# Kernel optimization log

Measured on AMD Instinct MI355X. Metric: run time of the kernel, lower is better.

The kernel has to match this reference:

```python
import jax, jax.numpy as jnp
import numpy as np

NUM_RAYS = 262144  # 512x512 image
NUM_SAMPLES = 64


def setup_inputs() -> dict:
    key = jax.random.key(0)
    k1, k2 = jax.random.split(key)
    rays_o = jax.random.normal(k1, (NUM_RAYS, 3), dtype=jnp.float32) * 0.1
    d = jax.random.normal(k2, (NUM_RAYS, 3), dtype=jnp.float32)
    rays_d = d / jnp.linalg.norm(d, axis=-1, keepdims=True)
    radii = jnp.full((1,), 1.3, dtype=jnp.float32)  # scene_radii buffer
    return {"rays_o": rays_o, "rays_d": rays_d, "radii": radii, "num_samples": NUM_SAMPLES}


def _raymarch_dense(rays_o, rays_d, radii, num_samples):
    # Ray-AABB (cube of half-extent radius) intersection + depth linspace.
    radius = radii[0]
    inv_d = 1.0 / jnp.where(rays_d == 0, jnp.full_like(rays_d, 1e-6), rays_d)
    off_neg = (-radius - rays_o) * inv_d
    off_pos = (radius - rays_o) * inv_d
    near = jnp.max(jnp.minimum(off_neg, off_pos), axis=-1, keepdims=True)  # [N,1]
    far = jnp.min(jnp.maximum(off_neg, off_pos), axis=-1, keepdims=True)   # [N,1]
    t = jnp.linspace(0.0, 1.0, num_samples, dtype=rays_o.dtype)[None]       # [1,S]
    depth = near + (far - near) * t                                         # [N,S]
    # perturb=False path (deterministic)
    samples = (rays_o[:, None, :] + rays_d[:, None, :] * depth[..., None]) / radius  # [N,S,3]
    deltas = jnp.diff(depth, axis=-1, prepend=near)                          # [N,S]
    # Concrete query_mask: occupied = inside unit sphere of normalized grid.
    mask = jnp.linalg.norm(samples, axis=-1) <= 1.0                          # [N,S] bool
    return samples, depth, deltas, mask


def reference(rays_o, rays_d, radii, num_samples):
    n = rays_o.shape[0]
    samples, depth, deltas, mask = _raymarch_dense(rays_o, rays_d, radii, num_samples)
    M = n * num_samples
    mf = mask.reshape(M)
    # Stable compaction: valid entries first, original order preserved (jnp.argsort is stable).
    order = jnp.argsort(jnp.logical_not(mf))
    num_valid = jnp.sum(mf).astype(jnp.int32)
    ridx_full = jnp.repeat(jnp.arange(n, dtype=jnp.int32), num_samples)
    ridx = ridx_full[order]                                  # [M]
    samples_c = samples.reshape(M, 3)[order]                 # [M,3]
    depth_c = depth.reshape(M)[order]                        # [M]
    deltas_c = deltas.reshape(M)[order][:, None]             # [M,1]
    valid = jnp.arange(M) < num_valid                        # padding indicator
    # mark_pack_boundaries: start of each per-ray pack
    boundary = jnp.concatenate([jnp.ones((1,), bool), ridx[1:] != ridx[:-1]]) & valid
    return ridx, samples_c, depth_c, deltas_c, boundary, num_valid
```

## Files before the change

### kernel.cpp

```cpp
#include <hip/hip_runtime.h>

#pragma clang fp contract(off)

namespace {

constexpr int S = 64;
constexpr float DELTA = 1.0f / 63.0f;

constexpr int RPB = 8;
constexpr int TPR = 256 / RPB;
constexpr int SPT = S / TPR;
constexpr int Q = RPB * S;
constexpr int LQ = Q + 16;
constexpr int SB = 4 * LQ;
constexpr int LDSF = SB + 3 * Q + 16;

__device__ __forceinline__ void ray_nearfar(
    float ox, float oy, float oz,
    float dx, float dy, float dz,
    float R, float& nr, float& fr) {
  float ix = 1.0f / ((dx == 0.0f) ? 1e-6f : dx);
  float iy = 1.0f / ((dy == 0.0f) ? 1e-6f : dy);
  float iz = 1.0f / ((dz == 0.0f) ? 1e-6f : dz);
  float mR = -R;
  float ax = (mR - ox) * ix, bx = (R - ox) * ix;
  float ay = (mR - oy) * iy, by = (R - oy) * iy;
  float az = (mR - oz) * iz, bz = (R - oz) * iz;
  nr = fmaxf(fmaxf(fminf(ax, bx), fminf(ay, by)), fminf(az, bz));
  fr = fminf(fminf(fmaxf(ax, bx), fmaxf(ay, by)), fmaxf(az, bz));
}

__global__ __launch_bounds__(256) void k_count(
    const float* __restrict__ ro, const float* __restrict__ rd,
    const float* __restrict__ radii,
    float4* __restrict__ rayinfo,
    int* __restrict__ L, int* __restrict__ blockSums, int N) {
  int r = blockIdx.x * 256 + threadIdx.x;
  int cnt = 0;
  const float QLIM = __uint_as_float(0x3F800001u);
  if (r < N) {
    float R = radii[0];
    float ox = ro[3 * r], oy = ro[3 * r + 1], oz = ro[3 * r + 2];
    float dx = rd[3 * r], dy = rd[3 * r + 1], dz = rd[3 * r + 2];
    float nr, fr;
    ray_nearfar(ox, oy, oz, dx, dy, dz, R, nr, fr);
    float f = fr - nr;
    unsigned lo = 0, hi = 0;
    for (int s = 0; s < S; ++s) {
      float dep = nr + f * ((float)s * DELTA);
      float sx = (ox + dx * dep) / R;
      float sy = (oy + dy * dep) / R;
      float sz = (oz + dz * dep) / R;
      float q = (sx * sx + sy * sy) + sz * sz;
      unsigned bit = (q <= QLIM) ? 1u : 0u;
      if (s < 32) lo |= bit << s; else hi |= bit << (s - 32);
      cnt += (int)bit;
    }
    rayinfo[r] = make_float4(nr, f, __uint_as_float(lo), __uint_as_float(hi));
  }
  __shared__ int sm[256];
  sm[threadIdx.x] = cnt;
  __syncthreads();
  for (int off = 1; off < 256; off <<= 1) {
    int t = (threadIdx.x >= off) ? sm[threadIdx.x - off] : 0;
    __syncthreads();
    sm[threadIdx.x] += t;
    __syncthreads();
  }
  if (r < N) L[r] = sm[threadIdx.x] - cnt;
  if (threadIdx.x == 255) blockSums[blockIdx.x] = sm[255];
}

__global__ __launch_bounds__(1024) void k_scan(
    const int* __restrict__ blockSums, int* __restrict__ blockOff,
    int* __restrict__ total, float* __restrict__ out_nv, int nb) {
  __shared__ int sm[1024];
  int x = (threadIdx.x < nb) ? blockSums[threadIdx.x] : 0;
  sm[threadIdx.x] = x;
  __syncthreads();
  for (int off = 1; off < 1024; off <<= 1) {
    int t = (threadIdx.x >= off) ? sm[threadIdx.x - off] : 0;
    __syncthreads();
    sm[threadIdx.x] += t;
    __syncthreads();
  }
  if (threadIdx.x < nb) blockOff[threadIdx.x] = sm[threadIdx.x] - x;
  if (threadIdx.x == 1023) {
    *total = sm[1023];
    out_nv[0] = (float)sm[1023];
  }
}

__global__ __launch_bounds__(256) void k_stage(
    const float* __restrict__ ro, const float* __restrict__ rd,
    const float* __restrict__ radii,
    const float4* __restrict__ rayinfo,
    const int* __restrict__ L, const int* __restrict__ blockOff,
    const int* __restrict__ total,
    float* __restrict__ out, int N) {
  __shared__ __align__(16) float buf[LDSF];
  int nwg = gridDim.x;
  int chunk = nwg >> 3;
  int hw = blockIdx.x;
  int bid = (hw & 7) * chunk + (hw >> 3);
  int r0 = bid * RPB;
  int tid = threadIdx.x;
  int nv = *total;
  int V0 = L[r0] + blockOff[r0 >> 8];
  int rB = r0 + RPB;
  int VB = (rB >= N) ? nv : (L[rB] + blockOff[rB >> 8]);
  int cV = VB - V0;
  int cT = Q - cV;
  int TV = r0 * S - V0;
  size_t tail0 = (size_t)nv + (size_t)TV;

  int sv = V0 & 3;
  int st = ((sv + cV + 3) & ~3) + (int)(tail0 & 3);
  int svS = (3 * V0) & 3;
  int stS = ((svS + 3 * cV + 3) & ~3) + (int)((3 * tail0) & 3);

  int r = r0 + (tid / TPR);
  float R = radii[0];
  float invR = 1.0f / R;
  float4 info = rayinfo[r];
  float nr = info.x, f = info.y;
  unsigned long long msk =
      ((unsigned long long)__float_as_uint(info.w) << 32) |
      (unsigned long long)__float_as_uint(info.z);
  float ox = ro[3 * r], oy = ro[3 * r + 1], oz = ro[3 * r + 2];
  float dx = rd[3 * r], dy = rd[3 * r + 1], dz = rd[3 * r + 2];
  int Vr = L[r] + blockOff[r >> 8];
  float fridx = (float)r;
  int idxvB = Vr - V0;
  int idxtB = (r * S - Vr) - TV;
  #pragma unroll
  for (int j = 0; j < SPT; ++j) {
    int s = (tid & (TPR - 1)) + TPR * j;
    bool bit = (msk >> s) & 1ull;
    int below = __popcll(msk & ((1ull << s) - 1ull));
    float dep = fmaf(f, (float)s * DELTA, nr);
    float sx = fmaf(dx, dep, ox) * invR;
    float sy = fmaf(dy, dep, oy) * invR;
    float sz = fmaf(dz, dep, oz) * invR;
    float prev = fmaf(f, (float)(s - 1) * DELTA, nr);
    float del = s ? (dep - prev) : 0.0f;
    int i1 = bit ? (idxvB + below) : (idxtB + (s - below));
    int b0 = (bit ? sv : st) + i1;
    buf[b0] = fridx;
    buf[b0 + LQ] = dep;
    buf[b0 + 2 * LQ] = del;
    buf[b0 + 3 * LQ] = (bit && below == 0) ? 1.0f : 0.0f;
    int b1 = SB + (bit ? svS : stS) + 3 * i1;
    buf[b1] = sx; buf[b1 + 1] = sy; buf[b1 + 2] = sz;
  }
  __syncthreads();

  size_t M = (size_t)N * S;
  const size_t A1 = 4 * M, A2 = 5 * M, A3 = 6 * M;

  {
    int a0 = (-V0) & 3; if (a0 > cV) a0 = cV;
    int body = cV - a0, n4 = body >> 2, rem = body & 3;
    int l0 = sv + a0;
    size_t g = (size_t)V0 + a0;
    for (int c = tid; c < n4; c += 256) {
      int l = l0 + 4 * c; size_t gg = g + 4 * (size_t)c;
      *(float4*)(out + gg)      = *(const float4*)&buf[l];
      *(float4*)(out + A1 + gg) = *(const float4*)&buf[l + LQ];
      *(float4*)(out + A2 + gg) = *(const float4*)&buf[l + 2 * LQ];
      *(float4*)(out + A3 + gg) = *(const float4*)&buf[l + 3 * LQ];
    }
    if (tid < a0) {
      size_t gg = (size_t)V0 + tid; int l = sv + tid;
      out[gg] = buf[l]; out[A1 + gg] = buf[l + LQ];
      out[A2 + gg] = buf[l + 2 * LQ]; out[A3 + gg] = buf[l + 3 * LQ];
    }
    if (tid < rem) {
      int e = a0 + 4 * n4 + tid;
      size_t gg = (size_t)V0 + e; int l = sv + e;
      out[gg] = buf[l]; out[A1 + gg] = buf[l + LQ];
      out[A2 + gg] = buf[l + 2 * LQ]; out[A3 + gg] = buf[l + 3 * LQ];
    }
  }
  {
    int a0 = (int)((-tail0) & 3); if (a0 > cT) a0 = cT;
    int body = cT - a0, n4 = body >> 2, rem = body & 3;
    int l0 = st + a0;
    size_t g = tail0 + a0;
    for (int c = tid; c < n4; c += 256) {
      int l = l0 + 4 * c; size_t gg = g + 4 * (size_t)c;
      *(float4*)(out + gg)      = *(const float4*)&buf[l];
      *(float4*)(out + A1 + gg) = *(const float4*)&buf[l + LQ];
      *(float4*)(out + A2 + gg) = *(const float4*)&buf[l + 2 * LQ];
      *(float4*)(out + A3 + gg) = *(const float4*)&buf[l + 3 * LQ];
    }
    if (tid < a0) {
      size_t gg = tail0 + tid; int l = st + tid;
      out[gg] = buf[l]; out[A1 + gg] = buf[l + LQ];
      out[A2 + gg] = buf[l + 2 * LQ]; out[A3 + gg] = buf[l + 3 * LQ];
    }
    if (tid < rem) {
      int e = a0 + 4 * n4 + tid;
      size_t gg = tail0 + e; int l = st + e;
      out[gg] = buf[l]; out[A1 + gg] = buf[l + LQ];
      out[A2 + gg] = buf[l + 2 * LQ]; out[A3 + gg] = buf[l + 3 * LQ];
    }
  }
  {
    size_t g0 = M + 3 * (size_t)V0; int cnt = 3 * cV;
    int a0 = (int)((-g0) & 3); if (a0 > cnt) a0 = cnt;
    int body = cnt - a0, n4 = body >> 2, rem = body & 3;
    int l0 = SB + svS + a0;
    for (int c = tid; c < n4; c += 256)
      *(float4*)(out + g0 + a0 + 4 * (size_t)c) = *(const float4*)&buf[l0 + 4 * c];
    if (tid < a0) out[g0 + tid] = buf[SB + svS + tid];
    if (tid < rem) { int e = a0 + 4 * n4 + tid; out[g0 + e] = buf[SB + svS + e]; }
  }
  {
    size_t g0 = M + 3 * tail0; int cnt = 3 * cT;
    int a0 = (int)((-g0) & 3); if (a0 > cnt) a0 = cnt;
    int body = cnt - a0, n4 = body >> 2, rem = body & 3;
    int l0 = SB + stS + a0;
    for (int c = tid; c < n4; c += 256)
      *(float4*)(out + g0 + a0 + 4 * (size_t)c) = *(const float4*)&buf[l0 + 4 * c];
    if (tid < a0) out[g0 + tid] = buf[SB + stS + tid];
    if (tid < rem) { int e = a0 + 4 * n4 + tid; out[g0 + e] = buf[SB + stS + e]; }
  }
}

}

extern "C" void kernel_launch(void* const* d_in, const int* in_sizes, int n_in,
                              void* d_out, int out_size, void* d_ws, size_t ws_size,
                              hipStream_t stream) {
  const float* ro = (const float*)d_in[0];
  const float* rd = (const float*)d_in[1];
  const float* radii = (const float*)d_in[2];
  int N = in_sizes[0] / 3;
  int M = N * S;
  int nbA = (N + 255) / 256;

  float4* rayinfo = (float4*)d_ws;
  int* wsI = (int*)(rayinfo + N);
  int* L = wsI;
  int* blockSums = wsI + N;
  int* blockOff = blockSums + nbA;
  int* total = blockOff + nbA;

  float* out = (float*)d_out;
  float* out_nv = out + (size_t)7 * (size_t)M;

  k_count<<<nbA, 256, 0, stream>>>(ro, rd, radii, rayinfo, L, blockSums, N);
  k_scan<<<1, 1024, 0, stream>>>(blockSums, blockOff, total, out_nv, nbA);
  k_stage<<<N / RPB, 256, 0, stream>>>(ro, rd, radii, rayinfo, L, blockOff,
                                       total, out, N);
}
```

Before: 139.1 us.

## Make staging kernel persistent with double-buffered LDS and prefetch; fast-path mask test

The staging kernel becomes persistent: 512 blocks each loop over several 16-ray chunks. Each block uses two LDS buffers and prefetches the next chunk's ray data while the current chunk is written out, to hide global load latency and cut launch and block-scheduling overhead. The count kernel now tests the sphere mask with FMA and a reciprocal multiply, and falls back to the exact division path only near the boundary, which reduces division cost. The risks are fewer resident blocks with larger LDS, losing the XCD-aware block remapping, and cpb truncation if the chunk count is not divisible by 512. The persistent loop also has a single barrier per chunk, so a chunk can overwrite the buffer from two chunks ago while slower threads may still be reading it.

```diff
diff --git a/kernel.cpp b/kernel.cpp
--- a/kernel.cpp
+++ b/kernel.cpp
@@ -7,13 +7,14 @@
 constexpr int S = 64;
 constexpr float DELTA = 1.0f / 63.0f;
 
-constexpr int RPB = 8;
+constexpr int RPB = 16;
 constexpr int TPR = 256 / RPB;
 constexpr int SPT = S / TPR;
 constexpr int Q = RPB * S;
 constexpr int LQ = Q + 16;
 constexpr int SB = 4 * LQ;
 constexpr int LDSF = SB + 3 * Q + 16;
+constexpr int NBLK = 512;
 
 __device__ __forceinline__ void ray_nearfar(
     float ox, float oy, float oz,
@@ -40,6 +41,7 @@
   const float QLIM = __uint_as_float(0x3F800001u);
   if (r < N) {
     float R = radii[0];
+    float invR = 1.0f / R;
     float ox = ro[3 * r], oy = ro[3 * r + 1], oz = ro[3 * r + 2];
     float dx = rd[3 * r], dy = rd[3 * r + 1], dz = rd[3 * r + 2];
     float nr, fr;
@@ -48,11 +50,20 @@
     unsigned lo = 0, hi = 0;
     for (int s = 0; s < S; ++s) {
       float dep = nr + f * ((float)s * DELTA);
-      float sx = (ox + dx * dep) / R;
-      float sy = (oy + dy * dep) / R;
-      float sz = (oz + dz * dep) / R;
-      float q = (sx * sx + sy * sy) + sz * sz;
-      unsigned bit = (q <= QLIM) ? 1u : 0u;
+      float sxf = fmaf(dx, dep, ox) * invR;
+      float syf = fmaf(dy, dep, oy) * invR;
+      float szf = fmaf(dz, dep, oz) * invR;
+      float qf = fmaf(sxf, sxf, fmaf(syf, syf, szf * szf));
+      unsigned bit;
+      if (__builtin_expect(fabsf(qf - 1.0f) > 6e-5f, 1)) {
+        bit = (qf <= 1.0f) ? 1u : 0u;
+      } else {
+        float sx = (ox + dx * dep) / R;
+        float sy = (oy + dy * dep) / R;
+        float sz = (oz + dz * dep) / R;
+        float q = (sx * sx + sy * sy) + sz * sz;
+        bit = (q <= QLIM) ? 1u : 0u;
+      }
       if (s < 32) lo |= bit << s; else hi |= bit << (s - 32);
       cnt += (int)bit;
     }
@@ -91,140 +102,162 @@
   }
 }
 
-__global__ __launch_bounds__(256) void k_stage(
+__global__ __launch_bounds__(256, 2) void k_stage(
     const float* __restrict__ ro, const float* __restrict__ rd,
     const float* __restrict__ radii,
     const float4* __restrict__ rayinfo,
     const int* __restrict__ L, const int* __restrict__ blockOff,
     const int* __restrict__ total,
-    float* __restrict__ out, int N) {
-  __shared__ __align__(16) float buf[LDSF];
-  int nwg = gridDim.x;
-  int chunk = nwg >> 3;
-  int hw = blockIdx.x;
-  int bid = (hw & 7) * chunk + (hw >> 3);
-  int r0 = bid * RPB;
-  int tid = threadIdx.x;
-  int nv = *total;
+    float* __restrict__ out, int N, int cpb) {
+  __shared__ __align__(16) float buf[2][LDSF];
+  const int tid = threadIdx.x;
+  const int nv = *total;
+  const float R = radii[0];
+  const float invR = 1.0f / R;
+  const size_t M = (size_t)N * S;
+  const size_t A1 = 4 * M, A2 = 5 * M, A3 = 6 * M;
+
+  int c0 = blockIdx.x * cpb;
+  int r0 = c0 * RPB;
   int V0 = L[r0] + blockOff[r0 >> 8];
   int rB = r0 + RPB;
   int VB = (rB >= N) ? nv : (L[rB] + blockOff[rB >> 8]);
-  int cV = VB - V0;
-  int cT = Q - cV;
-  int TV = r0 * S - V0;
-  size_t tail0 = (size_t)nv + (size_t)TV;
-
-  int sv = V0 & 3;
-  int st = ((sv + cV + 3) & ~3) + (int)(tail0 & 3);
-  int svS = (3 * V0) & 3;
-  int stS = ((svS + 3 * cV + 3) & ~3) + (int)((3 * tail0) & 3);
-
-  int r = r0 + (tid / TPR);
-  float R = radii[0];
-  float invR = 1.0f / R;
+  int r = r0 + (tid >> 4);
   float4 info = rayinfo[r];
-  float nr = info.x, f = info.y;
-  unsigned long long msk =
-      ((unsigned long long)__float_as_uint(info.w) << 32) |
-      (unsigned long long)__float_as_uint(info.z);
   float ox = ro[3 * r], oy = ro[3 * r + 1], oz = ro[3 * r + 2];
   float dx = rd[3 * r], dy = rd[3 * r + 1], dz = rd[3 * r + 2];
   int Vr = L[r] + blockOff[r >> 8];
-  float fridx = (float)r;
-  int idxvB = Vr - V0;
-  int idxtB = (r * S - Vr) - TV;
-  #pragma unroll
-  for (int j = 0; j < SPT; ++j) {
-    int s = (tid & (TPR - 1)) + TPR * j;
-    bool bit = (msk >> s) & 1ull;
-    int below = __popcll(msk & ((1ull << s) - 1ull));
-    float dep = fmaf(f, (float)s * DELTA, nr);
-    float sx = fmaf(dx, dep, ox) * invR;
-    float sy = fmaf(dy, dep, oy) * invR;
-    float sz = fmaf(dz, dep, oz) * invR;
-    float prev = fmaf(f, (float)(s - 1) * DELTA, nr);
-    float del = s ? (dep - prev) : 0.0f;
-    int i1 = bit ? (idxvB + below) : (idxtB + (s - below));
-    int b0 = (bit ? sv : st) + i1;
-    buf[b0] = fridx;
-    buf[b0 + LQ] = dep;
-    buf[b0 + 2 * LQ] = del;
-    buf[b0 + 3 * LQ] = (bit && below == 0) ? 1.0f : 0.0f;
-    int b1 = SB + (bit ? svS : stS) + 3 * i1;
-    buf[b1] = sx; buf[b1 + 1] = sy; buf[b1 + 2] = sz;
-  }
-  __syncthreads();
-
-  size_t M = (size_t)N * S;
-  const size_t A1 = 4 * M, A2 = 5 * M, A3 = 6 * M;
-
-  {
-    int a0 = (-V0) & 3; if (a0 > cV) a0 = cV;
-    int body = cV - a0, n4 = body >> 2, rem = body & 3;
-    int l0 = sv + a0;
-    size_t g = (size_t)V0 + a0;
-    for (int c = tid; c < n4; c += 256) {
-      int l = l0 + 4 * c; size_t gg = g + 4 * (size_t)c;
-      *(float4*)(out + gg)      = *(const float4*)&buf[l];
-      *(float4*)(out + A1 + gg) = *(const float4*)&buf[l + LQ];
-      *(float4*)(out + A2 + gg) = *(const float4*)&buf[l + 2 * LQ];
-      *(float4*)(out + A3 + gg) = *(const float4*)&buf[l + 3 * LQ];
-    }
-    if (tid < a0) {
-      size_t gg = (size_t)V0 + tid; int l = sv + tid;
-      out[gg] = buf[l]; out[A1 + gg] = buf[l + LQ];
-      out[A2 + gg] = buf[l + 2 * LQ]; out[A3 + gg] = buf[l + 3 * LQ];
-    }
-    if (tid < rem) {
-      int e = a0 + 4 * n4 + tid;
-      size_t gg = (size_t)V0 + e; int l = sv + e;
-      out[gg] = buf[l]; out[A1 + gg] = buf[l + LQ];
-      out[A2 + gg] = buf[l + 2 * LQ]; out[A3 + gg] = buf[l + 3 * LQ];
-    }
-  }
-  {
-    int a0 = (int)((-tail0) & 3); if (a0 > cT) a0 = cT;
-    int body = cT - a0, n4 = body >> 2, rem = body & 3;
-    int l0 = st + a0;
-    size_t g = tail0 + a0;
-    for (int c = tid; c < n4; c += 256) {
-      int l = l0 + 4 * c; size_t gg = g + 4 * (size_t)c;
-      *(float4*)(out + gg)      = *(const float4*)&buf[l];
-      *(float4*)(out + A1 + gg) = *(const float4*)&buf[l + LQ];
-      *(float4*)(out + A2 + gg) = *(const float4*)&buf[l + 2 * LQ];
-      *(float4*)(out + A3 + gg) = *(const float4*)&buf[l + 3 * LQ];
-    }
-    if (tid < a0) {
-      size_t gg = tail0 + tid; int l = st + tid;
-      out[gg] = buf[l]; out[A1 + gg] = buf[l + LQ];
-      out[A2 + gg] = buf[l + 2 * LQ]; out[A3 + gg] = buf[l + 3 * LQ];
-    }
-    if (tid < rem) {
-      int e = a0 + 4 * n4 + tid;
-      size_t gg = tail0 + e; int l = st + e;
-      out[gg] = buf[l]; out[A1 + gg] = buf[l + LQ];
-      out[A2 + gg] = buf[l + 2 * LQ]; out[A3 + gg] = buf[l + 3 * LQ];
-    }
-  }
-  {
-    size_t g0 = M + 3 * (size_t)V0; int cnt = 3 * cV;
-    int a0 = (int)((-g0) & 3); if (a0 > cnt) a0 = cnt;
-    int body = cnt - a0, n4 = body >> 2, rem = body & 3;
-    int l0 = SB + svS + a0;
-    for (int c = tid; c < n4; c += 256)
-      *(float4*)(out + g0 + a0 + 4 * (size_t)c) = *(const float4*)&buf[l0 + 4 * c];
-    if (tid < a0) out[g0 + tid] = buf[SB + svS + tid];
-    if (tid < rem) { int e = a0 + 4 * n4 + tid; out[g0 + e] = buf[SB + svS + e]; }
-  }
-  {
-    size_t g0 = M + 3 * tail0; int cnt = 3 * cT;
-    int a0 = (int)((-g0) & 3); if (a0 > cnt) a0 = cnt;
-    int body = cnt - a0, n4 = body >> 2, rem = body & 3;
-    int l0 = SB + stS + a0;
-    for (int c = tid; c < n4; c += 256)
-      *(float4*)(out + g0 + a0 + 4 * (size_t)c) = *(const float4*)&buf[l0 + 4 * c];
-    if (tid < a0) out[g0 + tid] = buf[SB + stS + tid];
-    if (tid < rem) { int e = a0 + 4 * n4 + tid; out[g0 + e] = buf[SB + stS + e]; }
+
+  for (int k = 0; k < cpb; ++k) {
+    float* bufp = buf[k & 1];
+    bool has_next = (k + 1 < cpb);
+    float4 n_info; float n_ox, n_oy, n_oz, n_dx, n_dy, n_dz;
+    int n_Vr = 0, n_VB = 0, n_r0 = 0;
+    if (has_next) {
+      n_r0 = (c0 + k + 1) * RPB;
+      int rr = n_r0 + (tid >> 4);
+      n_info = rayinfo[rr];
+      n_ox = ro[3 * rr]; n_oy = ro[3 * rr + 1]; n_oz = ro[3 * rr + 2];
+      n_dx = rd[3 * rr]; n_dy = rd[3 * rr + 1]; n_dz = rd[3 * rr + 2];
+      n_Vr = L[rr] + blockOff[rr >> 8];
+      int nrB = n_r0 + RPB;
+      n_VB = (nrB >= N) ? nv : (L[nrB] + blockOff[nrB >> 8]);
+    }
+
+    int cV = VB - V0;
+    int cT = Q - cV;
+    int TV = r0 * S - V0;
+    size_t tail0 = (size_t)nv + (size_t)TV;
+    int sv = V0 & 3;
+    int st = ((sv + cV + 3) & ~3) + (int)(tail0 & 3);
+    int svS = (3 * V0) & 3;
+    int stS = ((svS + 3 * cV + 3) & ~3) + (int)((3 * tail0) & 3);
+
+    float nr = info.x, f = info.y;
+    unsigned long long msk =
+        ((unsigned long long)__float_as_uint(info.w) << 32) |
+        (unsigned long long)__float_as_uint(info.z);
+    float fridx = (float)(r0 + (tid >> 4));
+    int rr = r0 + (tid >> 4);
+    int idxvB = Vr - V0;
+    int idxtB = (rr * S - Vr) - TV;
+    #pragma unroll
+    for (int j = 0; j < SPT; ++j) {
+      int s = (tid & (TPR - 1)) + TPR * j;
+      bool bit = (msk >> s) & 1ull;
+      int below = __popcll(msk & ((1ull << s) - 1ull));
+      float dep = fmaf(f, (float)s * DELTA, nr);
+      float sx = fmaf(dx, dep, ox) * invR;
+      float sy = fmaf(dy, dep, oy) * invR;
+      float sz = fmaf(dz, dep, oz) * invR;
+      float prev = fmaf(f, (float)(s - 1) * DELTA, nr);
+      float del = s ? (dep - prev) : 0.0f;
+      int i1 = bit ? (idxvB + below) : (idxtB + (s - below));
+      int b0 = (bit ? sv : st) + i1;
+      bufp[b0] = fridx;
+      bufp[b0 + LQ] = dep;
+      bufp[b0 + 2 * LQ] = del;
+      bufp[b0 + 3 * LQ] = (bit && below == 0) ? 1.0f : 0.0f;
+      int b1 = SB + (bit ? svS : stS) + 3 * i1;
+      bufp[b1] = sx; bufp[b1 + 1] = sy; bufp[b1 + 2] = sz;
+    }
+    __syncthreads();
+
+    {
+      int a0 = (-V0) & 3; if (a0 > cV) a0 = cV;
+      int body = cV - a0, n4 = body >> 2, rem = body & 3;
+      int l0 = sv + a0;
+      size_t g = (size_t)V0 + a0;
+      for (int c = tid; c < n4; c += 256) {
+        int l = l0 + 4 * c; size_t gg = g + 4 * (size_t)c;
+        *(float4*)(out + gg)      = *(const float4*)&bufp[l];
+        *(float4*)(out + A1 + gg) = *(const float4*)&bufp[l + LQ];
+        *(float4*)(out + A2 + gg) = *(const float4*)&bufp[l + 2 * LQ];
+        *(float4*)(out + A3 + gg) = *(const float4*)&bufp[l + 3 * LQ];
+      }
+      if (tid < a0) {
+        size_t gg = (size_t)V0 + tid; int l = sv + tid;
+        out[gg] = bufp[l]; out[A1 + gg] = bufp[l + LQ];
+        out[A2 + gg] = bufp[l + 2 * LQ]; out[A3 + gg] = bufp[l + 3 * LQ];
+      }
+      if (tid < rem) {
+        int e = a0 + 4 * n4 + tid;
+        size_t gg = (size_t)V0 + e; int l = sv + e;
+        out[gg] = bufp[l]; out[A1 + gg] = bufp[l + LQ];
+        out[A2 + gg] = bufp[l + 2 * LQ]; out[A3 + gg] = bufp[l + 3 * LQ];
+      }
+    }
+    {
+      int a0 = (int)((-tail0) & 3); if (a0 > cT) a0 = cT;
+      int body = cT - a0, n4 = body >> 2, rem = body & 3;
+      int l0 = st + a0;
+      size_t g = tail0 + a0;
+      for (int c = tid; c < n4; c += 256) {
+        int l = l0 + 4 * c; size_t gg = g + 4 * (size_t)c;
+        *(float4*)(out + gg)      = *(const float4*)&bufp[l];
+        *(float4*)(out + A1 + gg) = *(const float4*)&bufp[l + LQ];
+        *(float4*)(out + A2 + gg) = *(const float4*)&bufp[l + 2 * LQ];
+        *(float4*)(out + A3 + gg) = *(const float4*)&bufp[l + 3 * LQ];
+      }
+      if (tid < a0) {
+        size_t gg = tail0 + tid; int l = st + tid;
+        out[gg] = bufp[l]; out[A1 + gg] = bufp[l + LQ];
+        out[A2 + gg] = bufp[l + 2 * LQ]; out[A3 + gg] = bufp[l + 3 * LQ];
+      }
+      if (tid < rem) {
+        int e = a0 + 4 * n4 + tid;
+        size_t gg = tail0 + e; int l = st + e;
+        out[gg] = bufp[l]; out[A1 + gg] = bufp[l + LQ];
+        out[A2 + gg] = bufp[l + 2 * LQ]; out[A3 + gg] = bufp[l + 3 * LQ];
+      }
+    }
+    {
+      size_t g0 = M + 3 * (size_t)V0; int cnt = 3 * cV;
+      int a0 = (int)((-g0) & 3); if (a0 > cnt) a0 = cnt;
+      int body = cnt - a0, n4 = body >> 2, rem = body & 3;
+      int l0 = SB + svS + a0;
+      for (int c = tid; c < n4; c += 256)
+        *(float4*)(out + g0 + a0 + 4 * (size_t)c) = *(const float4*)&bufp[l0 + 4 * c];
+      if (tid < a0) out[g0 + tid] = bufp[SB + svS + tid];
+      if (tid < rem) { int e = a0 + 4 * n4 + tid; out[g0 + e] = bufp[SB + svS + e]; }
+    }
+    {
+      size_t g0 = M + 3 * tail0; int cnt = 3 * cT;
+      int a0 = (int)((-g0) & 3); if (a0 > cnt) a0 = cnt;
+      int body = cnt - a0, n4 = body >> 2, rem = body & 3;
+      int l0 = SB + stS + a0;
+      for (int c = tid; c < n4; c += 256)
+        *(float4*)(out + g0 + a0 + 4 * (size_t)c) = *(const float4*)&bufp[l0 + 4 * c];
+      if (tid < a0) out[g0 + tid] = bufp[SB + stS + tid];
+      if (tid < rem) { int e = a0 + 4 * n4 + tid; out[g0 + e] = bufp[SB + stS + e]; }
+    }
+
+    if (has_next) {
+      r0 = n_r0; V0 = VB; VB = n_VB;
+      info = n_info; Vr = n_Vr;
+      ox = n_ox; oy = n_oy; oz = n_oz;
+      dx = n_dx; dy = n_dy; dz = n_dz;
+    }
   }
 }
 
@@ -239,6 +272,8 @@
   int N = in_sizes[0] / 3;
   int M = N * S;
   int nbA = (N + 255) / 256;
+  int chunks = N / RPB;
+  int cpb = chunks / NBLK;
 
   float4* rayinfo = (float4*)d_ws;
   int* wsI = (int*)(rayinfo + N);
@@ -252,6 +287,6 @@
 
   k_count<<<nbA, 256, 0, stream>>>(ro, rd, radii, rayinfo, L, blockSums, N);
   k_scan<<<1, 1024, 0, stream>>>(blockSums, blockOff, total, out_nv, nbA);
-  k_stage<<<N / RPB, 256, 0, stream>>>(ro, rd, radii, rayinfo, L, blockOff,
-                                       total, out, N);
-}
+  k_stage<<<NBLK, 256, 0, stream>>>(ro, rd, radii, rayinfo, L, blockOff,
+                                    total, out, N, cpb);
+}
```

Result: slower. 154.9 us (+11.3%).

## Fuse block-sum scan into count kernel, add fast FMA mask test, double rays per block

Applied to the files above, without the earlier changes.

Removes the separate single-block scan kernel. The last count block to finish, detected through an atomic counter, now scans the block sums itself. The per-sample inside-sphere test uses FMA and a reciprocal multiply, falling back to the exact division path only when the value lies near the boundary. The staging kernel handles 16 rays per block instead of 8. This adds a memset launch, and the 256-thread last-block scan covers only up to 1024 block sums.

```diff
diff --git a/kernel.cpp b/kernel.cpp
--- a/kernel.cpp
+++ b/kernel.cpp
@@ -7,7 +7,7 @@
 constexpr int S = 64;
 constexpr float DELTA = 1.0f / 63.0f;
 
-constexpr int RPB = 8;
+constexpr int RPB = 16;
 constexpr int TPR = 256 / RPB;
 constexpr int SPT = S / TPR;
 constexpr int Q = RPB * S;
@@ -34,12 +34,15 @@
     const float* __restrict__ ro, const float* __restrict__ rd,
     const float* __restrict__ radii,
     float4* __restrict__ rayinfo,
-    int* __restrict__ L, int* __restrict__ blockSums, int N) {
+    int* __restrict__ L, int* __restrict__ blockSums,
+    int* __restrict__ blockOff, int* __restrict__ total,
+    float* __restrict__ out_nv, int* __restrict__ counter, int N) {
   int r = blockIdx.x * 256 + threadIdx.x;
   int cnt = 0;
   const float QLIM = __uint_as_float(0x3F800001u);
   if (r < N) {
     float R = radii[0];
+    float invR = 1.0f / R;
     float ox = ro[3 * r], oy = ro[3 * r + 1], oz = ro[3 * r + 2];
     float dx = rd[3 * r], dy = rd[3 * r + 1], dz = rd[3 * r + 2];
     float nr, fr;
@@ -48,11 +51,20 @@
     unsigned lo = 0, hi = 0;
     for (int s = 0; s < S; ++s) {
       float dep = nr + f * ((float)s * DELTA);
-      float sx = (ox + dx * dep) / R;
-      float sy = (oy + dy * dep) / R;
-      float sz = (oz + dz * dep) / R;
-      float q = (sx * sx + sy * sy) + sz * sz;
-      unsigned bit = (q <= QLIM) ? 1u : 0u;
+      float sxf = fmaf(dx, dep, ox) * invR;
+      float syf = fmaf(dy, dep, oy) * invR;
+      float szf = fmaf(dz, dep, oz) * invR;
+      float qf = fmaf(sxf, sxf, fmaf(syf, syf, szf * szf));
+      unsigned bit;
+      if (__builtin_expect(fabsf(qf - 1.0f) > 6e-5f, 1)) {
+        bit = (qf <= 1.0f) ? 1u : 0u;
+      } else {
+        float sx = (ox + dx * dep) / R;
+        float sy = (oy + dy * dep) / R;
+        float sz = (oz + dz * dep) / R;
+        float q = (sx * sx + sy * sy) + sz * sz;
+        bit = (q <= QLIM) ? 1u : 0u;
+      }
       if (s < 32) lo |= bit << s; else hi |= bit << (s - 32);
       cnt += (int)bit;
     }
@@ -69,25 +81,38 @@
   }
   if (r < N) L[r] = sm[threadIdx.x] - cnt;
   if (threadIdx.x == 255) blockSums[blockIdx.x] = sm[255];
-}
-
-__global__ __launch_bounds__(1024) void k_scan(
-    const int* __restrict__ blockSums, int* __restrict__ blockOff,
-    int* __restrict__ total, float* __restrict__ out_nv, int nb) {
-  __shared__ int sm[1024];
-  int x = (threadIdx.x < nb) ? blockSums[threadIdx.x] : 0;
-  sm[threadIdx.x] = x;
-  __syncthreads();
-  for (int off = 1; off < 1024; off <<= 1) {
-    int t = (threadIdx.x >= off) ? sm[threadIdx.x - off] : 0;
-    __syncthreads();
-    sm[threadIdx.x] += t;
-    __syncthreads();
-  }
-  if (threadIdx.x < nb) blockOff[threadIdx.x] = sm[threadIdx.x] - x;
-  if (threadIdx.x == 1023) {
-    *total = sm[1023];
-    out_nv[0] = (float)sm[1023];
+
+  __threadfence();
+  __shared__ int lastFlag;
+  if (threadIdx.x == 0)
+    lastFlag = (atomicAdd(counter, 1) == (int)gridDim.x - 1) ? 1 : 0;
+  __syncthreads();
+  if (!lastFlag) return;
+
+  int nb = (int)gridDim.x;
+  int base = threadIdx.x * 4;
+  int v0 = (base + 0 < nb) ? atomicAdd(&blockSums[base + 0], 0) : 0;
+  int v1 = (base + 1 < nb) ? atomicAdd(&blockSums[base + 1], 0) : 0;
+  int v2 = (base + 2 < nb) ? atomicAdd(&blockSums[base + 2], 0) : 0;
+  int v3 = (base + 3 < nb) ? atomicAdd(&blockSums[base + 3], 0) : 0;
+  int s1 = v0 + v1, s2 = s1 + v2, s3 = s2 + v3;
+  __shared__ int sm2[256];
+  sm2[threadIdx.x] = s3;
+  __syncthreads();
+  for (int off = 1; off < 256; off <<= 1) {
+    int t = (threadIdx.x >= off) ? sm2[threadIdx.x - off] : 0;
+    __syncthreads();
+    sm2[threadIdx.x] += t;
+    __syncthreads();
+  }
+  int excl = sm2[threadIdx.x] - s3;
+  if (base + 0 < nb) blockOff[base + 0] = excl;
+  if (base + 1 < nb) blockOff[base + 1] = excl + v0;
+  if (base + 2 < nb) blockOff[base + 2] = excl + s1;
+  if (base + 3 < nb) blockOff[base + 3] = excl + s2;
+  if (threadIdx.x == 255) {
+    *total = sm2[255];
+    out_nv[0] = (float)sm2[255];
   }
 }
 
@@ -119,7 +144,7 @@
   int svS = (3 * V0) & 3;
   int stS = ((svS + 3 * cV + 3) & ~3) + (int)((3 * tail0) & 3);
 
-  int r = r0 + (tid / TPR);
+  int r = r0 + (tid >> 4);
   float R = radii[0];
   float invR = 1.0f / R;
   float4 info = rayinfo[r];
@@ -246,12 +271,14 @@
   int* blockSums = wsI + N;
   int* blockOff = blockSums + nbA;
   int* total = blockOff + nbA;
+  int* counter = total + 1;
 
   float* out = (float*)d_out;
   float* out_nv = out + (size_t)7 * (size_t)M;
 
-  k_count<<<nbA, 256, 0, stream>>>(ro, rd, radii, rayinfo, L, blockSums, N);
-  k_scan<<<1, 1024, 0, stream>>>(blockSums, blockOff, total, out_nv, nbA);
+  hipMemsetAsync(counter, 0, sizeof(int), stream);
+  k_count<<<nbA, 256, 0, stream>>>(ro, rd, radii, rayinfo, L, blockSums,
+                                   blockOff, total, out_nv, counter, N);
   k_stage<<<N / RPB, 256, 0, stream>>>(ro, rd, radii, rayinfo, L, blockOff,
                                        total, out, N);
 }
```

New measurement: 200.1 us. +43.8%, slower.
